# Optimization experiments

Hardware: AMD Instinct MI355X
Metric: run time of the kernel (lower is better)

Reference implementation:

```python
import jax, jax.numpy as jnp
import numpy as np

B, T, N = 64, 256, 8192
D_EMB, D_ATT = 32, 128


def setup_inputs() -> dict:
    keys = iter(jax.random.split(jax.random.key(0), 64))
    nk = lambda: next(keys)
    inp = {}
    inp["x_ped"] = jax.random.normal(nk(), (B, T, 4), jnp.float32)
    inp["x_ego"] = jax.random.normal(nk(), (B, T, 4), jnp.float32)
    inp["h_ped"] = jax.random.normal(nk(), (B, D_EMB), jnp.float32)
    dims = {"neighbor": 4, "light": 6, "sign": 5, "crosswalk": 7, "station": 7}
    for name, d in dims.items():
        inp["x_" + name] = jax.random.normal(nk(), (N, T, d), jnp.float32)
        # class labels; -1 marks invalid/padded object at that timestep
        inp["cls_" + name] = jax.random.randint(nk(), (N, T), -1, 3, dtype=jnp.int32)
        inp["seg_" + name] = jnp.sort(jax.random.randint(nk(), (N,), 0, B, dtype=jnp.int32))

    def lin(din, dout):
        k1, k2 = jax.random.split(nk())
        return (jax.random.normal(k1, (din, dout), jnp.float32) / float(np.sqrt(din)),
                jax.random.normal(k2, (dout,), jnp.float32) * 0.01)

    inp["Wp"], inp["bp"] = lin(4, D_EMB)      # target_box_embedding
    inp["Wn"], inp["bn"] = lin(4, D_EMB)      # x_neighbor embedding
    inp["Wl"], inp["bl"] = lin(6, D_EMB)      # x_light
    inp["Wsi"], inp["bsi"] = lin(5, D_EMB)    # x_sign
    inp["Wc"], inp["bc"] = lin(7, D_EMB)      # x_crosswalk
    inp["Wst"], inp["bst"] = lin(7, D_EMB)    # x_station
    inp["We"], inp["be"] = lin(4, D_EMB)      # x_ego
    inp["Wax"], _ = lin(D_EMB, D_ATT)         # additive attention: value proj
    inp["Wah"], inp["ba"] = lin(D_EMB, D_ATT)  # additive attention: query proj
    inp["va"] = jax.random.normal(nk(), (D_ATT,), jnp.float32) / float(np.sqrt(D_ATT))
    inp["W1"], inp["b1"] = lin(7 * D_EMB, D_EMB)  # classifier (6 traffic types + ped)
    inp["W2"], inp["b2"] = lin(D_EMB, D_EMB)
    inp["W3"], inp["b3"] = lin(D_EMB, 1)
    inp["t"] = 8
    return inp


def _masked_segment_softmax(score, mask, seg, num_segments):
    # equals torch.exp(score)/segment_sum(exp) over valid objects, stably
    s = jnp.where(mask, score, -1e30)
    smax = jax.ops.segment_max(s, seg, num_segments=num_segments)
    smax = jnp.where(smax > -1e29, smax, 0.0)  # empty segments -> 0
    e = jnp.where(mask, jnp.exp(score - smax[seg]), 0.0)
    denom = jax.ops.segment_sum(e, seg, num_segments=num_segments)
    return e / jnp.maximum(denom[seg], 1e-30)


def _attend_type(x, cls, seg, W, b, h_ped, Wax, Wah, ba, va, t):
    emb_t = jax.nn.relu(x[:, t] @ W + b)                    # [N, 32]
    mask = cls[:, t] != -1                                   # [N]
    # additive attention score: v^T tanh(Wx*x + Wh*h + b)
    score = jnp.tanh(emb_t @ Wax + h_ped[seg] @ Wah + ba) @ va  # [N]
    probs = _masked_segment_softmax(score, mask, seg, B)     # [N], 0 where masked
    # identity-matmul scatter-add in the original == segment_sum
    feat = jax.ops.segment_sum(emb_t * probs[:, None], seg, num_segments=B)  # [B, 32]
    return feat, probs


def reference(x_ped, x_ego, h_ped,
              x_neighbor, cls_neighbor, seg_neighbor,
              x_light, cls_light, seg_light,
              x_sign, cls_sign, seg_sign,
              x_crosswalk, cls_crosswalk, seg_crosswalk,
              x_station, cls_station, seg_station,
              Wp, bp, Wn, bn, Wl, bl, Wsi, bsi, Wc, bc, Wst, bst, We, be,
              Wax, Wah, ba, va, W1, b1, W2, b2, W3, b3, t):
    ped_t = jax.nn.relu(x_ped[:, t] @ Wp + bp)               # [B, 32]
    ego_t = jax.nn.relu(x_ego[:, t] @ We + be)               # ego is a plain tensor (cls_ego is Tensor)
    f_n, p_n = _attend_type(x_neighbor, cls_neighbor, seg_neighbor, Wn, bn, h_ped, Wax, Wah, ba, va, t)
    f_l, p_l = _attend_type(x_light, cls_light, seg_light, Wl, bl, h_ped, Wax, Wah, ba, va, t)
    f_si, p_si = _attend_type(x_sign, cls_sign, seg_sign, Wsi, bsi, h_ped, Wax, Wah, ba, va, t)
    f_c, p_c = _attend_type(x_crosswalk, cls_crosswalk, seg_crosswalk, Wc, bc, h_ped, Wax, Wah, ba, va, t)
    f_st, p_st = _attend_type(x_station, cls_station, seg_station, Wst, bst, h_ped, Wax, Wah, ba, va, t)
    feats = jnp.concatenate([ped_t, f_n, f_l, f_si, f_c, f_st, ego_t], axis=-1)  # [B, 224]
    # classifier (dropout is identity in eval)
    h1 = jax.nn.relu(feats @ W1 + b1)
    h2 = jax.nn.relu(h1 @ W2 + b2)
    int_det_score = h2 @ W3 + b3                             # [B, 1]
    return int_det_score, feats, p_n, p_l, p_si, p_c, p_st
```

## Files before the change

### kernel.cpp

```cpp
#include <hip/hip_runtime.h>

#define TSTEPS 256
#define NOBJ   8192
#define BATCH  64
#define DEMB   32
#define DATT   128

#define HW_OFF     0
#define EX_OFF     32768
#define SEGOFF_OFF 196608
#define EMB_OFF    199168
#define WS_NEED    (EMB_OFF + 5 * NOBJ * DEMB * 4)

struct SP {
    const float* x[5]; const int* cls[5]; const int* seg[5];
    const float* W[5]; const float* bias[5];
    const float* x_ped; const float* x_ego; const float* h_ped;
    const float* Wp; const float* bp; const float* We; const float* be;
    const float* Wax; const float* Wah; const float* ba; const float* va;
    const float* W1; const float* b1; const float* W2; const float* b2;
    const float* W3; const float* b3;
    const int* t_ptr;
    float* out;
    float* hW;
    float* ex;
    int* seg_off;
    float* emb;
    int d[5];
    int use_emb;
};

__device__ __forceinline__ int load_t(const void* p) {
    unsigned w0 = *(const unsigned*)p;
    if (w0 < (unsigned)TSTEPS) return (int)w0;
    float f = __uint_as_float(w0);
    if (f >= 0.f && f < 256.f) return (int)f;
    return 8;
}

__device__ __forceinline__ float fast_tanh(float x) {
    float e = __expf(2.0f * x);
    return 1.0f - 2.0f / (e + 1.0f);
}

__global__ __launch_bounds__(256) void k_prep(SP p) {
    if (blockIdx.x >= BATCH) {
        const int g    = (blockIdx.x - BATCH) * 256 + threadIdx.x;
        const int type = g >> 13;
        const int i    = g & (NOBJ - 1);
        const int* __restrict__ seg = p.seg[type];
        const int sv = seg[i];
        const int pv = (i == 0) ? -1 : seg[i - 1];
        for (int v = pv + 1; v <= sv; ++v) p.seg_off[type * 65 + v] = i;
        if (i == NOBJ - 1)
            for (int v = sv + 1; v <= BATCH; ++v) p.seg_off[type * 65 + v] = NOBJ;
        return;
    }
    const int b = blockIdx.x;
    const int j = threadIdx.x;
    const int t = load_t(p.t_ptr);
    if (j < DATT) {
        float a = p.ba[j];
        const float* h = p.h_ped + b * DEMB;
        #pragma unroll
        for (int k = 0; k < DEMB; ++k) a += h[k] * p.Wah[k * DATT + j];
        p.hW[b * DATT + j] = a;
    }
    if (j < DEMB) {
        const float* xp = p.x_ped + (size_t)(b * TSTEPS + t) * 4;
        float e = p.bp[j];
        #pragma unroll
        for (int k = 0; k < 4; ++k) e += xp[k] * p.Wp[k * DEMB + j];
        p.out[64 + b * 224 + j] = fmaxf(e, 0.f);
        const float* xe = p.x_ego + (size_t)(b * TSTEPS + t) * 4;
        float g = p.be[j];
        #pragma unroll
        for (int k = 0; k < 4; ++k) g += xe[k] * p.We[k * DEMB + j];
        p.out[64 + b * 224 + 192 + j] = fmaxf(g, 0.f);
    }
}

#define EPAD 36
template<int D>
__device__ __forceinline__ void score_body(const SP& p, const int type, const int t,
                                           float* WaxT, float* embS) {
    const int tid = threadIdx.x;
    const float* __restrict__ x   = p.x[type];
    const int*   __restrict__ cls = p.cls[type];
    const int*   __restrict__ seg = p.seg[type];
    const int blkbase = blockIdx.x * 64;

    const int s = tid >> 4;
    const int q = tid & 15;

    int bseg[4], cv[4];
    #pragma unroll
    for (int po = 0; po < 4; ++po) {
        const int i = blkbase + s + 16 * po;
        bseg[po] = seg[i];
        cv[po]   = cls[i * TSTEPS + t];
    }

    for (int idx = tid; idx < DATT * DEMB; idx += 256) {
        const int j = idx >> 5, k = idx & 31;
        WaxT[idx] = p.Wax[k * DATT + j];
    }
    const float* __restrict__ Wt = p.W[type];
    const float* __restrict__ bt = p.bias[type];
    float* __restrict__ embg = p.emb + ((size_t)type * NOBJ + blkbase) * DEMB;
    for (int idx = tid; idx < 64 * DEMB; idx += 256) {
        const int o = idx >> 5, col = idx & 31;
        const float* xr = x + (size_t)((blkbase + o) * TSTEPS + t) * D;
        float a = bt[col];
        #pragma unroll
        for (int k = 0; k < D; ++k) a += xr[k] * Wt[k * DEMB + col];
        a = fmaxf(a, 0.f);
        embS[o * EPAD + col] = a;
        if (p.use_emb) embg[idx] = a;
    }
    __syncthreads();

    float acc[4][8];
    #pragma unroll
    for (int po = 0; po < 4; ++po)
        #pragma unroll
        for (int jo = 0; jo < 8; ++jo) acc[po][jo] = 0.f;

    #pragma unroll
    for (int cc = 0; cc < 8; ++cc) {
        const int ch = (cc + q) & 7;
        const float4 e0 = *(const float4*)&embS[(s     ) * EPAD + 4 * ch];
        const float4 e1 = *(const float4*)&embS[(s + 16) * EPAD + 4 * ch];
        const float4 e2 = *(const float4*)&embS[(s + 32) * EPAD + 4 * ch];
        const float4 e3 = *(const float4*)&embS[(s + 48) * EPAD + 4 * ch];
        #pragma unroll
        for (int jo = 0; jo < 8; ++jo) {
            const float4 w = *(const float4*)&WaxT[(q * 8 + jo) * DEMB + 4 * ch];
            acc[0][jo] += e0.x*w.x + e0.y*w.y + e0.z*w.z + e0.w*w.w;
            acc[1][jo] += e1.x*w.x + e1.y*w.y + e1.z*w.z + e1.w*w.w;
            acc[2][jo] += e2.x*w.x + e2.y*w.y + e2.z*w.z + e2.w*w.w;
            acc[3][jo] += e3.x*w.x + e3.y*w.y + e3.z*w.z + e3.w*w.w;
        }
    }

    float vv[8];
    *(float4*)(vv)     = *(const float4*)(p.va + q * 8);
    *(float4*)(vv + 4) = *(const float4*)(p.va + q * 8 + 4);
    float sc[4];
    #pragma unroll
    for (int po = 0; po < 4; ++po) {
        float hv[8];
        const float* hp = p.hW + bseg[po] * DATT + q * 8;
        *(float4*)(hv)     = *(const float4*)(hp);
        *(float4*)(hv + 4) = *(const float4*)(hp + 4);
        float v = 0.f;
        #pragma unroll
        for (int jo = 0; jo < 8; ++jo)
            v += fast_tanh(hv[jo] + acc[po][jo]) * vv[jo];
        sc[po] = v;
    }
    #pragma unroll
    for (int po = 0; po < 4; ++po) {
        sc[po] += __shfl_xor(sc[po], 1);
        sc[po] += __shfl_xor(sc[po], 2);
        sc[po] += __shfl_xor(sc[po], 4);
        sc[po] += __shfl_xor(sc[po], 8);
    }
    if (q == 0) {
        #pragma unroll
        for (int po = 0; po < 4; ++po)
            p.ex[type * NOBJ + blkbase + s + 16 * po] = (cv[po] != -1) ? __expf(sc[po]) : 0.f;
    }
}

__global__ __launch_bounds__(256) void k_score(SP p) {
    __shared__ __align__(16) float WaxT[DATT * DEMB];
    __shared__ __align__(16) float embS[64 * EPAD];
    const int t = load_t(p.t_ptr);
    switch (blockIdx.y) {
        case 0: score_body<4>(p, 0, t, WaxT, embS); break;
        case 1: score_body<6>(p, 1, t, WaxT, embS); break;
        case 2: score_body<5>(p, 2, t, WaxT, embS); break;
        case 3: score_body<7>(p, 3, t, WaxT, embS); break;
        default: score_body<7>(p, 4, t, WaxT, embS); break;
    }
}

__global__ __launch_bounds__(256) void k_finish(SP p) {
    const int type = blockIdx.y;
    const int bseg = blockIdx.x;
    const int tid  = threadIdx.x;
    const int j    = tid & 31;
    const int sl   = tid >> 5;
    const int wv   = tid >> 6;
    const float* __restrict__ ex = p.ex + type * NOBJ;
    const int lo = p.seg_off[type * 65 + bseg];
    const int hi = p.seg_off[type * 65 + bseg + 1];

    __shared__ float red4[4];
    __shared__ float ared[4][DEMB];

    float s = 0.f;
    for (int i = lo + tid; i < hi; i += 256) s += ex[i];
    #pragma unroll
    for (int off = 32; off; off >>= 1) s += __shfl_xor(s, off);
    if ((tid & 63) == 0) red4[wv] = s;
    __syncthreads();
    const float inv = 1.0f / fmaxf(red4[0] + red4[1] + red4[2] + red4[3], 1e-30f);

    float acc = 0.f;
    float* pout = p.out + 64 + BATCH * 224 + type * NOBJ;
    if (p.use_emb) {
        const float* __restrict__ eb = p.emb + (size_t)type * NOBJ * DEMB;
        for (int i = lo + sl; i < hi; i += 8) {
            const float pr = ex[i] * inv;
            if (j == 0) pout[i] = pr;
            acc += pr * eb[(size_t)i * DEMB + j];
        }
    } else {
        const int t = load_t(p.t_ptr);
        const int d = p.d[type];
        float wj[7];
        for (int k = 0; k < d; ++k) wj[k] = p.W[type][k * DEMB + j];
        const float bj = p.bias[type][j];
        for (int i = lo + sl; i < hi; i += 8) {
            const float e = ex[i];
            const float pr = e * inv;
            if (j == 0) pout[i] = pr;
            if (e > 0.f) {
                const float* xr = p.x[type] + (size_t)(i * TSTEPS + t) * d;
                float a = bj;
                for (int k = 0; k < d; ++k) a += xr[k] * wj[k];
                acc += pr * fmaxf(a, 0.f);
            }
        }
    }
    acc += __shfl_xor(acc, 32);
    if ((tid & 63) < 32) ared[wv][j] = acc;
    __syncthreads();
    if (tid < DEMB) {
        const float f = ared[0][tid] + ared[1][tid] + ared[2][tid] + ared[3][tid];
        p.out[64 + bseg * 224 + 32 * (1 + type) + tid] = f;
    }
}

__global__ __launch_bounds__(64) void k_head(SP p) {
    const int b   = blockIdx.x;
    const int tid = threadIdx.x;
    const int j    = tid & 31;
    const int half = tid >> 5;
    __shared__ float h1s[DEMB];
    __shared__ float h2s[DEMB];
    const float* feats = p.out + 64 + b * 224;

    float a = 0.f;
    const int k0 = half * 112;
    #pragma unroll 4
    for (int k = k0; k < k0 + 112; ++k)
        a += feats[k] * p.W1[k * DEMB + j];
    a += __shfl_xor(a, 32);
    if (half == 0) h1s[j] = fmaxf(a + p.b1[j], 0.f);
    __syncthreads();

    float a2 = 0.f;
    const int k2 = half * 16;
    #pragma unroll
    for (int k = k2; k < k2 + 16; ++k)
        a2 += h1s[k] * p.W2[k * DEMB + j];
    a2 += __shfl_xor(a2, 32);
    if (half == 0) h2s[j] = fmaxf(a2 + p.b2[j], 0.f);
    __syncthreads();

    if (half == 0) {
        float v = h2s[j] * p.W3[j];
        v += __shfl_xor(v, 16); v += __shfl_xor(v, 8);
        v += __shfl_xor(v, 4);  v += __shfl_xor(v, 2); v += __shfl_xor(v, 1);
        if (j == 0) p.out[b] = v + p.b3[0];
    }
}

extern "C" void kernel_launch(void* const* d_in, const int* in_sizes, int n_in,
                              void* d_out, int out_size, void* d_ws, size_t ws_size,
                              hipStream_t stream) {
    (void)in_sizes; (void)n_in; (void)out_size;

    SP p;
    const int xi[5] = {3, 6, 9, 12, 15};
    const int wi[5] = {20, 22, 24, 26, 28};
    const int di[5] = {4, 6, 5, 7, 7};
    for (int tp = 0; tp < 5; ++tp) {
        p.x[tp]    = (const float*)d_in[xi[tp]];
        p.cls[tp]  = (const int*)d_in[xi[tp] + 1];
        p.seg[tp]  = (const int*)d_in[xi[tp] + 2];
        p.W[tp]    = (const float*)d_in[wi[tp]];
        p.bias[tp] = (const float*)d_in[wi[tp] + 1];
        p.d[tp]    = di[tp];
    }
    p.x_ped = (const float*)d_in[0];
    p.x_ego = (const float*)d_in[1];
    p.h_ped = (const float*)d_in[2];
    p.Wp = (const float*)d_in[18]; p.bp = (const float*)d_in[19];
    p.We = (const float*)d_in[30]; p.be = (const float*)d_in[31];
    p.Wax = (const float*)d_in[32]; p.Wah = (const float*)d_in[33];
    p.ba  = (const float*)d_in[34]; p.va  = (const float*)d_in[35];
    p.W1 = (const float*)d_in[36]; p.b1 = (const float*)d_in[37];
    p.W2 = (const float*)d_in[38]; p.b2 = (const float*)d_in[39];
    p.W3 = (const float*)d_in[40]; p.b3 = (const float*)d_in[41];
    p.t_ptr = (const int*)d_in[42];
    p.out = (float*)d_out;
    char* ws = (char*)d_ws;
    p.hW      = (float*)(ws + HW_OFF);
    p.ex      = (float*)(ws + EX_OFF);
    p.seg_off = (int*)(ws + SEGOFF_OFF);
    p.emb     = (float*)(ws + EMB_OFF);
    p.use_emb = (ws_size >= (size_t)WS_NEED) ? 1 : 0;

    hipLaunchKernelGGL(k_prep,   dim3(BATCH + 160),  dim3(256), 0, stream, p);
    hipLaunchKernelGGL(k_score,  dim3(NOBJ / 64, 5), dim3(256), 0, stream, p);
    hipLaunchKernelGGL(k_finish, dim3(BATCH, 5),     dim3(256), 0, stream, p);
    hipLaunchKernelGGL(k_head,   dim3(BATCH),        dim3(64),  0, stream, p);
}
```

Baseline: 45.21 us.

## Fuse prep into score kernel and merge finish with classifier head

Removes the separate prep kernel: segment offsets are computed inside the score blocks, and each block recomputes the query projection hW for the segments it covers into shared memory, with a fallback for spans beyond 32 segments. The finish and head kernels are merged into one per-batch kernel that loops over the five types, computes the ped/ego embeddings, and runs the MLP from shared features. This cuts four launches to two and drops global round-trips, at the cost of redundant hW computation per score block, more shared memory, and less parallelism in the finish stage (64 blocks instead of 320).

After: 129.7 us. +186.8%, slower.

```diff
diff --git a/kernel.cpp b/kernel.cpp
--- a/kernel.cpp
+++ b/kernel.cpp
@@ -6,10 +6,9 @@
 #define DEMB   32
 #define DATT   128
 
-#define HW_OFF     0
-#define EX_OFF     32768
-#define SEGOFF_OFF 196608
-#define EMB_OFF    199168
+#define EX_OFF     0
+#define SEGOFF_OFF 163840
+#define EMB_OFF    166400
 #define WS_NEED    (EMB_OFF + 5 * NOBJ * DEMB * 4)
 
 struct SP {
@@ -22,7 +21,6 @@
     const float* W3; const float* b3;
     const int* t_ptr;
     float* out;
-    float* hW;
     float* ex;
     int* seg_off;
     float* emb;
@@ -43,56 +41,31 @@
     return 1.0f - 2.0f / (e + 1.0f);
 }
 
-__global__ __launch_bounds__(256) void k_prep(SP p) {
-    if (blockIdx.x >= BATCH) {
-        const int g    = (blockIdx.x - BATCH) * 256 + threadIdx.x;
-        const int type = g >> 13;
-        const int i    = g & (NOBJ - 1);
-        const int* __restrict__ seg = p.seg[type];
+#define EPAD 36
+#define HWSPAN 32
+template<int D>
+__device__ __forceinline__ void score_body(const SP& p, const int type, const int t,
+                                           float* WaxT, float* embS, float* hWl) {
+    const int tid = threadIdx.x;
+    const float* __restrict__ x   = p.x[type];
+    const int*   __restrict__ cls = p.cls[type];
+    const int*   __restrict__ seg = p.seg[type];
+    const int blkbase = blockIdx.x * 64;
+
+    const int s = tid >> 4;
+    const int q = tid & 15;
+
+    if (tid < 64) {
+        const int i  = blkbase + tid;
         const int sv = seg[i];
         const int pv = (i == 0) ? -1 : seg[i - 1];
         for (int v = pv + 1; v <= sv; ++v) p.seg_off[type * 65 + v] = i;
         if (i == NOBJ - 1)
             for (int v = sv + 1; v <= BATCH; ++v) p.seg_off[type * 65 + v] = NOBJ;
-        return;
-    }
-    const int b = blockIdx.x;
-    const int j = threadIdx.x;
-    const int t = load_t(p.t_ptr);
-    if (j < DATT) {
-        float a = p.ba[j];
-        const float* h = p.h_ped + b * DEMB;
-        #pragma unroll
-        for (int k = 0; k < DEMB; ++k) a += h[k] * p.Wah[k * DATT + j];
-        p.hW[b * DATT + j] = a;
-    }
-    if (j < DEMB) {
-        const float* xp = p.x_ped + (size_t)(b * TSTEPS + t) * 4;
-        float e = p.bp[j];
-        #pragma unroll
-        for (int k = 0; k < 4; ++k) e += xp[k] * p.Wp[k * DEMB + j];
-        p.out[64 + b * 224 + j] = fmaxf(e, 0.f);
-        const float* xe = p.x_ego + (size_t)(b * TSTEPS + t) * 4;
-        float g = p.be[j];
-        #pragma unroll
-        for (int k = 0; k < 4; ++k) g += xe[k] * p.We[k * DEMB + j];
-        p.out[64 + b * 224 + 192 + j] = fmaxf(g, 0.f);
-    }
-}
-
-#define EPAD 36
-template<int D>
-__device__ __forceinline__ void score_body(const SP& p, const int type, const int t,
-                                           float* WaxT, float* embS) {
-    const int tid = threadIdx.x;
-    const float* __restrict__ x   = p.x[type];
-    const int*   __restrict__ cls = p.cls[type];
-    const int*   __restrict__ seg = p.seg[type];
-    const int blkbase = blockIdx.x * 64;
-
-    const int s = tid >> 4;
-    const int q = tid & 15;
-
+    }
+
+    const int sfirst = seg[blkbase];
+    const int slast  = seg[blkbase + 63];
     int bseg[4], cv[4];
     #pragma unroll
     for (int po = 0; po < 4; ++po) {
@@ -104,6 +77,16 @@
     for (int idx = tid; idx < DATT * DEMB; idx += 256) {
         const int j = idx >> 5, k = idx & 31;
         WaxT[idx] = p.Wax[k * DATT + j];
+    }
+    const int nseg = min(slast - sfirst + 1, HWSPAN);
+    for (int e2 = tid; e2 < nseg * DATT; e2 += 256) {
+        const int sidx = sfirst + (e2 >> 7);
+        const int j = e2 & 127;
+        float a = p.ba[j];
+        const float* h = p.h_ped + sidx * DEMB;
+        #pragma unroll
+        for (int k = 0; k < DEMB; ++k) a += h[k] * p.Wah[k * DATT + j];
+        hWl[(e2 >> 7) * DATT + j] = a;
     }
     const float* __restrict__ Wt = p.W[type];
     const float* __restrict__ bt = p.bias[type];
@@ -149,10 +132,22 @@
     float sc[4];
     #pragma unroll
     for (int po = 0; po < 4; ++po) {
+        const int rel = bseg[po] - sfirst;
         float hv[8];
-        const float* hp = p.hW + bseg[po] * DATT + q * 8;
-        *(float4*)(hv)     = *(const float4*)(hp);
-        *(float4*)(hv + 4) = *(const float4*)(hp + 4);
+        if (rel < HWSPAN) {
+            const float* hp = hWl + rel * DATT + q * 8;
+            *(float4*)(hv)     = *(const float4*)(hp);
+            *(float4*)(hv + 4) = *(const float4*)(hp + 4);
+        } else {
+            #pragma unroll
+            for (int jo = 0; jo < 8; ++jo) {
+                const int j = q * 8 + jo;
+                float a = p.ba[j];
+                const float* h = p.h_ped + bseg[po] * DEMB;
+                for (int k = 0; k < DEMB; ++k) a += h[k] * p.Wah[k * DATT + j];
+                hv[jo] = a;
+            }
+        }
         float v = 0.f;
         #pragma unroll
         for (int jo = 0; jo < 8; ++jo)
@@ -176,106 +171,121 @@
 __global__ __launch_bounds__(256) void k_score(SP p) {
     __shared__ __align__(16) float WaxT[DATT * DEMB];
     __shared__ __align__(16) float embS[64 * EPAD];
+    __shared__ __align__(16) float hWl[HWSPAN * DATT];
     const int t = load_t(p.t_ptr);
     switch (blockIdx.y) {
-        case 0: score_body<4>(p, 0, t, WaxT, embS); break;
-        case 1: score_body<6>(p, 1, t, WaxT, embS); break;
-        case 2: score_body<5>(p, 2, t, WaxT, embS); break;
-        case 3: score_body<7>(p, 3, t, WaxT, embS); break;
-        default: score_body<7>(p, 4, t, WaxT, embS); break;
-    }
-}
-
-__global__ __launch_bounds__(256) void k_finish(SP p) {
-    const int type = blockIdx.y;
-    const int bseg = blockIdx.x;
-    const int tid  = threadIdx.x;
-    const int j    = tid & 31;
-    const int sl   = tid >> 5;
-    const int wv   = tid >> 6;
-    const float* __restrict__ ex = p.ex + type * NOBJ;
-    const int lo = p.seg_off[type * 65 + bseg];
-    const int hi = p.seg_off[type * 65 + bseg + 1];
-
+        case 0: score_body<4>(p, 0, t, WaxT, embS, hWl); break;
+        case 1: score_body<6>(p, 1, t, WaxT, embS, hWl); break;
+        case 2: score_body<5>(p, 2, t, WaxT, embS, hWl); break;
+        case 3: score_body<7>(p, 3, t, WaxT, embS, hWl); break;
+        default: score_body<7>(p, 4, t, WaxT, embS, hWl); break;
+    }
+}
+
+__global__ __launch_bounds__(256) void k_fin(SP p) {
+    const int b   = blockIdx.x;
+    const int tid = threadIdx.x;
+    const int j   = tid & 31;
+    const int sl  = tid >> 5;
+    const int wv  = tid >> 6;
+    const int t   = load_t(p.t_ptr);
+
+    __shared__ float feats_s[224];
     __shared__ float red4[4];
     __shared__ float ared[4][DEMB];
-
-    float s = 0.f;
-    for (int i = lo + tid; i < hi; i += 256) s += ex[i];
-    #pragma unroll
-    for (int off = 32; off; off >>= 1) s += __shfl_xor(s, off);
-    if ((tid & 63) == 0) red4[wv] = s;
-    __syncthreads();
-    const float inv = 1.0f / fmaxf(red4[0] + red4[1] + red4[2] + red4[3], 1e-30f);
-
-    float acc = 0.f;
-    float* pout = p.out + 64 + BATCH * 224 + type * NOBJ;
-    if (p.use_emb) {
-        const float* __restrict__ eb = p.emb + (size_t)type * NOBJ * DEMB;
-        for (int i = lo + sl; i < hi; i += 8) {
-            const float pr = ex[i] * inv;
-            if (j == 0) pout[i] = pr;
-            acc += pr * eb[(size_t)i * DEMB + j];
-        }
-    } else {
-        const int t = load_t(p.t_ptr);
-        const int d = p.d[type];
-        float wj[7];
-        for (int k = 0; k < d; ++k) wj[k] = p.W[type][k * DEMB + j];
-        const float bj = p.bias[type][j];
-        for (int i = lo + sl; i < hi; i += 8) {
-            const float e = ex[i];
-            const float pr = e * inv;
-            if (j == 0) pout[i] = pr;
-            if (e > 0.f) {
-                const float* xr = p.x[type] + (size_t)(i * TSTEPS + t) * d;
-                float a = bj;
-                for (int k = 0; k < d; ++k) a += xr[k] * wj[k];
-                acc += pr * fmaxf(a, 0.f);
+    __shared__ float h1s[DEMB], h2s[DEMB];
+
+    if (tid < 64) {
+        const bool ego = tid >= 32;
+        const float* xr = (ego ? p.x_ego : p.x_ped) + (size_t)(b * TSTEPS + t) * 4;
+        const float* W  = ego ? p.We : p.Wp;
+        const float* bb = ego ? p.be : p.bp;
+        float a = bb[j];
+        #pragma unroll
+        for (int k = 0; k < 4; ++k) a += xr[k] * W[k * DEMB + j];
+        a = fmaxf(a, 0.f);
+        const int col = ego ? 192 + j : j;
+        feats_s[col] = a;
+        p.out[64 + b * 224 + col] = a;
+    }
+
+    for (int type = 0; type < 5; ++type) {
+        const float* __restrict__ ex = p.ex + type * NOBJ;
+        const int lo = p.seg_off[type * 65 + b];
+        const int hi = p.seg_off[type * 65 + b + 1];
+
+        float s = 0.f;
+        for (int i = lo + tid; i < hi; i += 256) s += ex[i];
+        #pragma unroll
+        for (int off = 32; off; off >>= 1) s += __shfl_xor(s, off);
+        if ((tid & 63) == 0) red4[wv] = s;
+        __syncthreads();
+        const float inv = 1.0f / fmaxf(red4[0] + red4[1] + red4[2] + red4[3], 1e-30f);
+
+        float acc = 0.f;
+        float* pout = p.out + 64 + BATCH * 224 + type * NOBJ;
+        if (p.use_emb) {
+            const float* __restrict__ eb = p.emb + (size_t)type * NOBJ * DEMB;
+            for (int i = lo + sl; i < hi; i += 8) {
+                const float pr = ex[i] * inv;
+                if (j == 0) pout[i] = pr;
+                acc += pr * eb[(size_t)i * DEMB + j];
+            }
+        } else {
+            const int d = p.d[type];
+            float wj[7];
+            for (int k = 0; k < d; ++k) wj[k] = p.W[type][k * DEMB + j];
+            const float bj = p.bias[type][j];
+            for (int i = lo + sl; i < hi; i += 8) {
+                const float e = ex[i];
+                const float pr = e * inv;
+                if (j == 0) pout[i] = pr;
+                if (e > 0.f) {
+                    const float* xr = p.x[type] + (size_t)(i * TSTEPS + t) * d;
+                    float a = bj;
+                    for (int k = 0; k < d; ++k) a += xr[k] * wj[k];
+                    acc += pr * fmaxf(a, 0.f);
+                }
             }
         }
-    }
-    acc += __shfl_xor(acc, 32);
-    if ((tid & 63) < 32) ared[wv][j] = acc;
+        acc += __shfl_xor(acc, 32);
+        __syncthreads();
+        if ((tid & 63) < 32) ared[wv][j] = acc;
+        __syncthreads();
+        if (tid < DEMB) {
+            const float f = ared[0][tid] + ared[1][tid] + ared[2][tid] + ared[3][tid];
+            feats_s[32 + type * 32 + tid] = f;
+            p.out[64 + b * 224 + 32 * (1 + type) + tid] = f;
+        }
+    }
+    __syncthreads();
+
+    float a1 = 0.f;
+    {
+        const int k0 = sl * 28;
+        #pragma unroll 4
+        for (int k = k0; k < k0 + 28; ++k)
+            a1 += feats_s[k] * p.W1[k * DEMB + j];
+    }
+    a1 += __shfl_xor(a1, 32);
+    __syncthreads();
+    if ((tid & 63) < 32) ared[wv][j] = a1;
+    __syncthreads();
+    if (tid < DEMB)
+        h1s[tid] = fmaxf(ared[0][tid] + ared[1][tid] + ared[2][tid] + ared[3][tid] + p.b1[tid], 0.f);
     __syncthreads();
     if (tid < DEMB) {
-        const float f = ared[0][tid] + ared[1][tid] + ared[2][tid] + ared[3][tid];
-        p.out[64 + bseg * 224 + 32 * (1 + type) + tid] = f;
-    }
-}
-
-__global__ __launch_bounds__(64) void k_head(SP p) {
-    const int b   = blockIdx.x;
-    const int tid = threadIdx.x;
-    const int j    = tid & 31;
-    const int half = tid >> 5;
-    __shared__ float h1s[DEMB];
-    __shared__ float h2s[DEMB];
-    const float* feats = p.out + 64 + b * 224;
-
-    float a = 0.f;
-    const int k0 = half * 112;
-    #pragma unroll 4
-    for (int k = k0; k < k0 + 112; ++k)
-        a += feats[k] * p.W1[k * DEMB + j];
-    a += __shfl_xor(a, 32);
-    if (half == 0) h1s[j] = fmaxf(a + p.b1[j], 0.f);
-    __syncthreads();
-
-    float a2 = 0.f;
-    const int k2 = half * 16;
-    #pragma unroll
-    for (int k = k2; k < k2 + 16; ++k)
-        a2 += h1s[k] * p.W2[k * DEMB + j];
-    a2 += __shfl_xor(a2, 32);
-    if (half == 0) h2s[j] = fmaxf(a2 + p.b2[j], 0.f);
-    __syncthreads();
-
-    if (half == 0) {
-        float v = h2s[j] * p.W3[j];
+        float a2 = p.b2[tid];
+        #pragma unroll
+        for (int k = 0; k < DEMB; ++k) a2 += h1s[k] * p.W2[k * DEMB + tid];
+        h2s[tid] = fmaxf(a2, 0.f);
+    }
+    __syncthreads();
+    if (tid < DEMB) {
+        float v = h2s[tid] * p.W3[tid];
         v += __shfl_xor(v, 16); v += __shfl_xor(v, 8);
         v += __shfl_xor(v, 4);  v += __shfl_xor(v, 2); v += __shfl_xor(v, 1);
-        if (j == 0) p.out[b] = v + p.b3[0];
+        if (tid == 0) p.out[b] = v + p.b3[0];
     }
 }
 
@@ -309,14 +319,11 @@
     p.t_ptr = (const int*)d_in[42];
     p.out = (float*)d_out;
     char* ws = (char*)d_ws;
-    p.hW      = (float*)(ws + HW_OFF);
     p.ex      = (float*)(ws + EX_OFF);
     p.seg_off = (int*)(ws + SEGOFF_OFF);
     p.emb     = (float*)(ws + EMB_OFF);
     p.use_emb = (ws_size >= (size_t)WS_NEED) ? 1 : 0;
 
-    hipLaunchKernelGGL(k_prep,   dim3(BATCH + 160),  dim3(256), 0, stream, p);
-    hipLaunchKernelGGL(k_score,  dim3(NOBJ / 64, 5), dim3(256), 0, stream, p);
-    hipLaunchKernelGGL(k_finish, dim3(BATCH, 5),     dim3(256), 0, stream, p);
-    hipLaunchKernelGGL(k_head,   dim3(BATCH),        dim3(64),  0, stream, p);
-}
+    hipLaunchKernelGGL(k_score, dim3(NOBJ / 64, 5), dim3(256), 0, stream, p);
+    hipLaunchKernelGGL(k_fin,   dim3(BATCH),        dim3(256), 0, stream, p);
+}
```
